# Kernel tuning notes

Measured on AMD Instinct MI355X. Metric: run time of the kernel, lower is better.

## Reference

```python
import jax, jax.numpy as jnp
import numpy as np

VOCAB = 32000
D = 256
B, S = 16, 128


def setup_inputs() -> dict:
    key = jax.random.key(0)
    ks = jax.random.split(key, 8)
    s = 1.0 / np.sqrt(D)
    return {
        "X": jax.random.randint(ks[0], (B, S), 0, VOCAB),
        "emb": jax.random.normal(ks[1], (VOCAB, D), dtype=jnp.float32),
        "Wl": jax.random.uniform(ks[2], (D, D), jnp.float32, -s, s),
        "bl": jax.random.uniform(ks[3], (D,), jnp.float32, -s, s),
        "Wr": jax.random.uniform(ks[4], (D, D), jnp.float32, -s, s),
        "br": jax.random.uniform(ks[5], (D,), jnp.float32, -s, s),
        "Wrel": jax.random.uniform(ks[6], (D, D), jnp.float32, -s, s),
        "brel": jax.random.uniform(ks[7], (D,), jnp.float32, -s, s),
    }


def reference(X, emb, Wl, bl, Wr, br, Wrel, brel):
    # X: [B,S] int -> embed [B,S,D]
    e = emb[X]
    L = jnp.einsum("bsd,de->bse", e, Wl.T) + bl  # left projection per token
    R = jnp.einsum("bsd,de->bse", e, Wr.T) + br  # right projection per token
    # all-pairs relu(L_i + R_j): [B,S,S,D]
    pair = jax.nn.relu(L[:, :, None, :] + R[:, None, :, :])
    # relation is affine, so mean over S^2 pairs commutes with it (same math,
    # one [B,D] GEMM instead of B*S^2 tiny ones)
    pooled = pair.mean(axis=(1, 2))  # [B,D]
    return pooled @ Wrel.T + brel
```

## Files before the change

kernel.cpp:

```cpp
#include <hip/hip_runtime.h>
#include <hip/hip_bf16.h>

#define DD 256
#define SS 128
#define BB 16

typedef __attribute__((ext_vector_type(8))) short bf16x8;
typedef __attribute__((ext_vector_type(4))) short bf16x4;
typedef __attribute__((ext_vector_type(4))) float f32x4;

static __device__ __forceinline__ short f2bf(float f) {
    __hip_bfloat16 h = __float2bfloat16(f);
    return *reinterpret_cast<short*>(&h);
}

static __device__ __forceinline__ int swz_off(int r, int kb) {
    return r * 512 + (kb ^ ((r & 7) << 4) ^ (((r >> 3) & 3) << 7));
}


__global__ __launch_bounds__(256) void k_proj(
    const int* __restrict__ X, const float* __restrict__ emb,
    const float* __restrict__ Wl, const float* __restrict__ bl,
    const float* __restrict__ Wr, const float* __restrict__ br,
    float* __restrict__ Lsd, float* __restrict__ Rsd,
    float* __restrict__ sumLp, float* __restrict__ sumRp)
{
    __shared__ __align__(16) short Ebf[64 * 256];
    __shared__ __align__(16) short Wbf[32 * 256];
    __shared__ float redw[4 * 16];
    __shared__ int toks[64];

    const int tid = threadIdx.x;
    const int bx  = blockIdx.x;
    const int tc  = bx >> 4;
    const int cc  = bx & 15;
    const int b   = tc >> 1;
    const int s0  = (tc & 1) * 64;
    const float* Wsrc = (cc < 8) ? Wl : Wr;
    const float* bsrc = (cc < 8) ? bl : br;
    const int dr0 = (cc & 7) * 32;

    if (tid < 64) toks[tid] = X[b * SS + s0 + tid];
    __syncthreads();

    char* Eb = (char*)Ebf;
    char* Wb = (char*)Wbf;

#pragma unroll
    for (int i = 0; i < 16; ++i) {
        int v = i * 256 + tid;
        int row = v >> 6, c4 = v & 63;
        float4 f = *(const float4*)&emb[(size_t)toks[row] * DD + c4 * 4];
        bf16x4 p; p[0] = f2bf(f.x); p[1] = f2bf(f.y); p[2] = f2bf(f.z); p[3] = f2bf(f.w);
        *(bf16x4*)(Eb + swz_off(row, c4 * 8)) = p;
    }
#pragma unroll
    for (int i = 0; i < 8; ++i) {
        int v = i * 256 + tid;
        int row = v >> 6, c4 = v & 63;
        float4 f = *(const float4*)&Wsrc[(size_t)(dr0 + row) * DD + c4 * 4];
        bf16x4 p; p[0] = f2bf(f.x); p[1] = f2bf(f.y); p[2] = f2bf(f.z); p[3] = f2bf(f.w);
        *(bf16x4*)(Wb + swz_off(row, c4 * 8)) = p;
    }
    __syncthreads();

    const int w    = tid >> 6;
    const int lane = tid & 63;
    const int wm = w >> 1, wn = w & 1;
    const int lr = lane & 15, lk = lane >> 4;

    f32x4 acc0 = {0.f, 0.f, 0.f, 0.f}, acc1 = acc0;
#pragma unroll
    for (int ks = 0; ks < 8; ++ks) {
        const int kb = ks * 64 + lk * 16;
        bf16x8 a0 = *(bf16x8*)(Eb + swz_off(wm * 32 + lr,      kb));
        bf16x8 a1 = *(bf16x8*)(Eb + swz_off(wm * 32 + 16 + lr, kb));
        bf16x8 b0 = *(bf16x8*)(Wb + swz_off(wn * 16 + lr,      kb));
        acc0 = __builtin_amdgcn_mfma_f32_16x16x32_bf16(a0, b0, acc0, 0, 0, 0);
        acc1 = __builtin_amdgcn_mfma_f32_16x16x32_bf16(a1, b0, acc1, 0, 0, 0);
    }

    const float bv = bsrc[dr0 + wn * 16 + lr];
    float* Tb = (cc < 8) ? Lsd : Rsd;
    const int dcol = dr0 + wn * 16 + lr;
#pragma unroll
    for (int reg = 0; reg < 4; ++reg) {
        int st = s0 + wm * 32 + lk * 4 + reg;
        Tb[((size_t)(b * SS) + st)      * DD + dcol] = acc0[reg] + bv;
        Tb[((size_t)(b * SS) + st + 16) * DD + dcol] = acc1[reg] + bv;
    }

    float t8 = (acc0[0] + acc0[1] + acc0[2] + acc0[3]) + bv * 8.0f
             + (acc1[0] + acc1[1] + acc1[2] + acc1[3]);
    t8 += __shfl_xor(t8, 16);
    t8 += __shfl_xor(t8, 32);
    if (lane < 16) redw[w * 16 + lr] = t8;
    __syncthreads();
    if (tid < 32) {
        int wn2 = tid >> 4, c = tid & 15;
        float s = redw[(0 * 2 + wn2) * 16 + c] + redw[(1 * 2 + wn2) * 16 + c];
        float* sp = (cc < 8) ? sumLp : sumRp;
        sp[(b * 2 + (tc & 1)) * DD + dr0 + wn2 * 16 + c] = s;
    }
}

__global__ __launch_bounds__(256) void k_pairs(
    const float* __restrict__ Lsd, const float* __restrict__ Rsd,
    float* __restrict__ absP)
{
    __shared__ float Ll[64 * 33];
    __shared__ float Rl[64 * 129];
    __shared__ float red[256];
    const int tid = threadIdx.x;
    const int bx  = blockIdx.x;
    const int b   = bx >> 4;
    const int dc  = (bx >> 2) & 3;
    const int is  = bx & 3;

#pragma unroll
    for (int it = 0; it < 2; ++it) {
        int v = it * 256 + tid;
        int srow = v >> 4, c4 = v & 15;
        float4 x = *(const float4*)&Lsd[((size_t)(b * SS) + is * 32 + srow) * DD + dc * 64 + c4 * 4];
        Ll[(c4 * 4 + 0) * 33 + srow] = x.x;
        Ll[(c4 * 4 + 1) * 33 + srow] = x.y;
        Ll[(c4 * 4 + 2) * 33 + srow] = x.z;
        Ll[(c4 * 4 + 3) * 33 + srow] = x.w;
    }
#pragma unroll
    for (int it = 0; it < 8; ++it) {
        int v = it * 256 + tid;
        int j = v >> 4, c4 = v & 15;
        float4 x = *(const float4*)&Rsd[((size_t)(b * SS) + j) * DD + dc * 64 + c4 * 4];
        Rl[(c4 * 4 + 0) * 129 + j] = x.x;
        Rl[(c4 * 4 + 1) * 129 + j] = x.y;
        Rl[(c4 * 4 + 2) * 129 + j] = x.z;
        Rl[(c4 * 4 + 3) * 129 + j] = x.w;
    }
    __syncthreads();

    const int dl = tid & 63;
    const int jg = tid >> 6;
    float rr[32];
#pragma unroll
    for (int j = 0; j < 32; ++j) rr[j] = Rl[dl * 129 + jg * 32 + j];

    float a0 = 0.f, a1 = 0.f, a2 = 0.f, a3 = 0.f;
#pragma unroll
    for (int i = 0; i < 32; ++i) {
        float l = Ll[dl * 33 + i];
#pragma unroll
        for (int j = 0; j < 32; j += 4) {
            a0 += fabsf(l + rr[j + 0]);
            a1 += fabsf(l + rr[j + 1]);
            a2 += fabsf(l + rr[j + 2]);
            a3 += fabsf(l + rr[j + 3]);
        }
    }
    red[tid] = (a0 + a1) + (a2 + a3);
    __syncthreads();
    if (tid < 64) {
        float s = red[tid] + red[tid + 64] + red[tid + 128] + red[tid + 192];
        absP[((b * 4 + dc) * 4 + is) * 64 + tid] = s;
    }
}

__global__ __launch_bounds__(256) void k_final(
    const float* __restrict__ sumLp, const float* __restrict__ sumRp,
    const float* __restrict__ absP,
    const float* __restrict__ Wrel, const float* __restrict__ brel,
    float* __restrict__ out)
{
    __shared__ float plds[DD];
    const int tid = threadIdx.x;
    const int b   = blockIdx.x;

    float sl = sumLp[(b * 2 + 0) * DD + tid] + sumLp[(b * 2 + 1) * DD + tid];
    float sr = sumRp[(b * 2 + 0) * DD + tid] + sumRp[(b * 2 + 1) * DD + tid];

    const int dc = tid >> 6, dl = tid & 63;
    float sa = 0.f;
#pragma unroll
    for (int is = 0; is < 4; ++is)
        sa += absP[((b * 4 + dc) * 4 + is) * 64 + dl];

    plds[tid] = (128.0f * (sl + sr) + sa) * (1.0f / 32768.0f);
    __syncthreads();

    float acc = brel[tid];
    const float4* w4 = (const float4*)(Wrel + (size_t)tid * DD);
#pragma unroll
    for (int k4 = 0; k4 < DD / 4; ++k4) {
        float4 p = *(float4*)&plds[k4 * 4];
        float4 w = w4[k4];
        acc = fmaf(p.x, w.x, acc);
        acc = fmaf(p.y, w.y, acc);
        acc = fmaf(p.z, w.z, acc);
        acc = fmaf(p.w, w.w, acc);
    }
    out[b * DD + tid] = acc;
}

extern "C" void kernel_launch(void* const* d_in, const int* in_sizes, int n_in,
                              void* d_out, int out_size, void* d_ws, size_t ws_size,
                              hipStream_t stream) {
    const int*   X    = (const int*)d_in[0];
    const float* emb  = (const float*)d_in[1];
    const float* Wl   = (const float*)d_in[2];
    const float* bl   = (const float*)d_in[3];
    const float* Wr   = (const float*)d_in[4];
    const float* br   = (const float*)d_in[5];
    const float* Wrel = (const float*)d_in[6];
    const float* brel = (const float*)d_in[7];
    float* out = (float*)d_out;

    float* ws = (float*)d_ws;
    float* Lsd   = ws;
    float* Rsd   = Lsd + (size_t)BB * SS * DD;
    float* sumLp = Rsd + (size_t)BB * SS * DD;
    float* sumRp = sumLp + BB * 2 * DD;
    float* absP  = sumRp + BB * 2 * DD;

    k_proj<<<512, 256, 0, stream>>>(X, emb, Wl, bl, Wr, br,
                                    Lsd, Rsd, sumLp, sumRp);
    k_pairs<<<256, 256, 0, stream>>>(Lsd, Rsd, absP);
    k_final<<<BB, 256, 0, stream>>>(sumLp, sumRp, absP, Wrel, brel, out);
}
```

Before: 29.63 us.

## Pre-convert embeddings and weights to bf16 once; store projections as bf16

Adds a conversion kernel that gathers the embedding rows and converts both projection weight matrices to bf16 in global memory once. k_proj then streams MFMA operands straight from global memory instead of having each of its 512 blocks re-convert fp32 data into swizzled LDS. The L/R projection outputs are stored as bf16, which halves the traffic into k_pairs. The cost is an extra kernel launch and lower precision in L/R for the abs-sum term.

```diff
diff --git a/kernel.cpp b/kernel.cpp
--- a/kernel.cpp
+++ b/kernel.cpp
@@ -6,89 +6,96 @@
 #define BB 16
 
 typedef __attribute__((ext_vector_type(8))) short bf16x8;
-typedef __attribute__((ext_vector_type(4))) short bf16x4;
 typedef __attribute__((ext_vector_type(4))) float f32x4;
 
 static __device__ __forceinline__ short f2bf(float f) {
     __hip_bfloat16 h = __float2bfloat16(f);
     return *reinterpret_cast<short*>(&h);
 }
-
-static __device__ __forceinline__ int swz_off(int r, int kb) {
-    return r * 512 + (kb ^ ((r & 7) << 4) ^ (((r >> 3) & 3) << 7));
-}
-
+static __device__ __forceinline__ float bf2f(short s) {
+    unsigned int u = ((unsigned int)(unsigned short)s) << 16;
+    return __uint_as_float(u);
+}
+
+
+__global__ __launch_bounds__(256) void k_conv(
+    const int* __restrict__ X, const float* __restrict__ emb,
+    const float* __restrict__ Wl, const float* __restrict__ Wr,
+    short* __restrict__ Ebfg, short* __restrict__ Wbfg)
+{
+    __shared__ int toksh[8];
+    const int tid = threadIdx.x;
+    const int bx  = blockIdx.x;
+    const int row = tid >> 5, g = tid & 31;
+
+    if (bx < 256) {
+        const int t0 = bx * 8;
+        if (tid < 8) toksh[tid] = X[t0 + tid];
+        __syncthreads();
+        const float* src = emb + (size_t)toksh[row] * DD + g * 8;
+        float4 f0 = *(const float4*)(src);
+        float4 f1 = *(const float4*)(src + 4);
+        bf16x8 p;
+        p[0]=f2bf(f0.x); p[1]=f2bf(f0.y); p[2]=f2bf(f0.z); p[3]=f2bf(f0.w);
+        p[4]=f2bf(f1.x); p[5]=f2bf(f1.y); p[6]=f2bf(f1.z); p[7]=f2bf(f1.w);
+        *(bf16x8*)(Ebfg + (size_t)(t0 + row) * DD + g * 8) = p;
+    } else {
+        const int w = (bx - 256) * 8 + row;
+        const float* src = ((w < 256) ? (Wl + (size_t)w * DD)
+                                      : (Wr + (size_t)(w - 256) * DD)) + g * 8;
+        float4 f0 = *(const float4*)(src);
+        float4 f1 = *(const float4*)(src + 4);
+        bf16x8 p;
+        p[0]=f2bf(f0.x); p[1]=f2bf(f0.y); p[2]=f2bf(f0.z); p[3]=f2bf(f0.w);
+        p[4]=f2bf(f1.x); p[5]=f2bf(f1.y); p[6]=f2bf(f1.z); p[7]=f2bf(f1.w);
+        *(bf16x8*)(Wbfg + (size_t)w * DD + g * 8) = p;
+    }
+}
 
 __global__ __launch_bounds__(256) void k_proj(
-    const int* __restrict__ X, const float* __restrict__ emb,
-    const float* __restrict__ Wl, const float* __restrict__ bl,
-    const float* __restrict__ Wr, const float* __restrict__ br,
-    float* __restrict__ Lsd, float* __restrict__ Rsd,
+    const short* __restrict__ Ebfg, const short* __restrict__ Wbfg,
+    const float* __restrict__ bl, const float* __restrict__ br,
+    short* __restrict__ Lsdh, short* __restrict__ Rsdh,
     float* __restrict__ sumLp, float* __restrict__ sumRp)
 {
-    __shared__ __align__(16) short Ebf[64 * 256];
-    __shared__ __align__(16) short Wbf[32 * 256];
     __shared__ float redw[4 * 16];
-    __shared__ int toks[64];
-
     const int tid = threadIdx.x;
     const int bx  = blockIdx.x;
     const int tc  = bx >> 4;
     const int cc  = bx & 15;
     const int b   = tc >> 1;
     const int s0  = (tc & 1) * 64;
-    const float* Wsrc = (cc < 8) ? Wl : Wr;
-    const float* bsrc = (cc < 8) ? bl : br;
+    const int t0  = tc * 64;
+    const int mat = cc >> 3;
     const int dr0 = (cc & 7) * 32;
-
-    if (tid < 64) toks[tid] = X[b * SS + s0 + tid];
-    __syncthreads();
-
-    char* Eb = (char*)Ebf;
-    char* Wb = (char*)Wbf;
-
-#pragma unroll
-    for (int i = 0; i < 16; ++i) {
-        int v = i * 256 + tid;
-        int row = v >> 6, c4 = v & 63;
-        float4 f = *(const float4*)&emb[(size_t)toks[row] * DD + c4 * 4];
-        bf16x4 p; p[0] = f2bf(f.x); p[1] = f2bf(f.y); p[2] = f2bf(f.z); p[3] = f2bf(f.w);
-        *(bf16x4*)(Eb + swz_off(row, c4 * 8)) = p;
-    }
-#pragma unroll
-    for (int i = 0; i < 8; ++i) {
-        int v = i * 256 + tid;
-        int row = v >> 6, c4 = v & 63;
-        float4 f = *(const float4*)&Wsrc[(size_t)(dr0 + row) * DD + c4 * 4];
-        bf16x4 p; p[0] = f2bf(f.x); p[1] = f2bf(f.y); p[2] = f2bf(f.z); p[3] = f2bf(f.w);
-        *(bf16x4*)(Wb + swz_off(row, c4 * 8)) = p;
-    }
-    __syncthreads();
 
     const int w    = tid >> 6;
     const int lane = tid & 63;
     const int wm = w >> 1, wn = w & 1;
     const int lr = lane & 15, lk = lane >> 4;
 
-    f32x4 acc0 = {0.f, 0.f, 0.f, 0.f}, acc1 = acc0;
+    const short* Arow0 = Ebfg + (size_t)(t0 + wm * 32 + lr) * DD + lk * 8;
+    const short* Arow1 = Arow0 + 16 * DD;
+    const short* Brow  = Wbfg + (size_t)(mat * 256 + dr0 + wn * 16 + lr) * DD + lk * 8;
+
+    f32x4 acc0 = {0.f,0.f,0.f,0.f}, acc1 = acc0;
 #pragma unroll
     for (int ks = 0; ks < 8; ++ks) {
-        const int kb = ks * 64 + lk * 16;
-        bf16x8 a0 = *(bf16x8*)(Eb + swz_off(wm * 32 + lr,      kb));
-        bf16x8 a1 = *(bf16x8*)(Eb + swz_off(wm * 32 + 16 + lr, kb));
-        bf16x8 b0 = *(bf16x8*)(Wb + swz_off(wn * 16 + lr,      kb));
+        bf16x8 a0 = *(const bf16x8*)(Arow0 + ks * 32);
+        bf16x8 a1 = *(const bf16x8*)(Arow1 + ks * 32);
+        bf16x8 b0 = *(const bf16x8*)(Brow  + ks * 32);
         acc0 = __builtin_amdgcn_mfma_f32_16x16x32_bf16(a0, b0, acc0, 0, 0, 0);
         acc1 = __builtin_amdgcn_mfma_f32_16x16x32_bf16(a1, b0, acc1, 0, 0, 0);
     }
 
-    const float bv = bsrc[dr0 + wn * 16 + lr];
-    float* Tb = (cc < 8) ? Lsd : Rsd;
+    const float bv = ((mat == 0) ? bl : br)[dr0 + wn * 16 + lr];
+    short* Tb = (mat == 0) ? Lsdh : Rsdh;
     const int dcol = dr0 + wn * 16 + lr;
 #pragma unroll
     for (int reg = 0; reg < 4; ++reg) {
         int st = s0 + wm * 32 + lk * 4 + reg;
-        Tb[((size_t)(b * SS) + st)      * DD + dcol] = acc0[reg] + bv;
-        Tb[((size_t)(b * SS) + st + 16) * DD + dcol] = acc1[reg] + bv;
+        Tb[((size_t)(b * SS) + st)      * DD + dcol] = f2bf(acc0[reg] + bv);
+        Tb[((size_t)(b * SS) + st + 16) * DD + dcol] = f2bf(acc1[reg] + bv);
     }
 
     float t8 = (acc0[0] + acc0[1] + acc0[2] + acc0[3]) + bv * 8.0f
@@ -100,13 +107,13 @@
     if (tid < 32) {
         int wn2 = tid >> 4, c = tid & 15;
         float s = redw[(0 * 2 + wn2) * 16 + c] + redw[(1 * 2 + wn2) * 16 + c];
-        float* sp = (cc < 8) ? sumLp : sumRp;
+        float* sp = (mat == 0) ? sumLp : sumRp;
         sp[(b * 2 + (tc & 1)) * DD + dr0 + wn2 * 16 + c] = s;
     }
 }
 
 __global__ __launch_bounds__(256) void k_pairs(
-    const float* __restrict__ Lsd, const float* __restrict__ Rsd,
+    const short* __restrict__ Lsdh, const short* __restrict__ Rsdh,
     float* __restrict__ absP)
 {
     __shared__ float Ll[64 * 33];
@@ -118,25 +125,19 @@
     const int dc  = (bx >> 2) & 3;
     const int is  = bx & 3;
 
-#pragma unroll
-    for (int it = 0; it < 2; ++it) {
+    {
+        int srow = tid >> 3, c8 = tid & 7;
+        bf16x8 x = *(const bf16x8*)&Lsdh[((size_t)(b * SS) + is * 32 + srow) * DD + dc * 64 + c8 * 8];
+#pragma unroll
+        for (int q = 0; q < 8; ++q) Ll[(c8 * 8 + q) * 33 + srow] = bf2f(x[q]);
+    }
+#pragma unroll
+    for (int it = 0; it < 4; ++it) {
         int v = it * 256 + tid;
-        int srow = v >> 4, c4 = v & 15;
-        float4 x = *(const float4*)&Lsd[((size_t)(b * SS) + is * 32 + srow) * DD + dc * 64 + c4 * 4];
-        Ll[(c4 * 4 + 0) * 33 + srow] = x.x;
-        Ll[(c4 * 4 + 1) * 33 + srow] = x.y;
-        Ll[(c4 * 4 + 2) * 33 + srow] = x.z;
-        Ll[(c4 * 4 + 3) * 33 + srow] = x.w;
-    }
-#pragma unroll
-    for (int it = 0; it < 8; ++it) {
-        int v = it * 256 + tid;
-        int j = v >> 4, c4 = v & 15;
-        float4 x = *(const float4*)&Rsd[((size_t)(b * SS) + j) * DD + dc * 64 + c4 * 4];
-        Rl[(c4 * 4 + 0) * 129 + j] = x.x;
-        Rl[(c4 * 4 + 1) * 129 + j] = x.y;
-        Rl[(c4 * 4 + 2) * 129 + j] = x.z;
-        Rl[(c4 * 4 + 3) * 129 + j] = x.w;
+        int j = v >> 3, c8 = v & 7;
+        bf16x8 x = *(const bf16x8*)&Rsdh[((size_t)(b * SS) + j) * DD + dc * 64 + c8 * 8];
+#pragma unroll
+        for (int q = 0; q < 8; ++q) Rl[(c8 * 8 + q) * 129 + j] = bf2f(x[q]);
     }
     __syncthreads();
 
@@ -215,15 +216,17 @@
     const float* brel = (const float*)d_in[7];
     float* out = (float*)d_out;
 
-    float* ws = (float*)d_ws;
-    float* Lsd   = ws;
-    float* Rsd   = Lsd + (size_t)BB * SS * DD;
-    float* sumLp = Rsd + (size_t)BB * SS * DD;
-    float* sumRp = sumLp + BB * 2 * DD;
-    float* absP  = sumRp + BB * 2 * DD;
-
-    k_proj<<<512, 256, 0, stream>>>(X, emb, Wl, bl, Wr, br,
-                                    Lsd, Rsd, sumLp, sumRp);
-    k_pairs<<<256, 256, 0, stream>>>(Lsd, Rsd, absP);
+    char* base = (char*)d_ws;
+    short* Ebfg  = (short*)(base);
+    short* Wbfg  = (short*)(base + (1u << 20));
+    short* Lsdh  = (short*)(base + 1310720);
+    short* Rsdh  = (short*)(base + 2359296);
+    float* sumLp = (float*)(base + 3407872);
+    float* sumRp = (float*)(base + 3440640);
+    float* absP  = (float*)(base + 3473408);
+
+    k_conv<<<320, 256, 0, stream>>>(X, emb, Wl, Wr, Ebfg, Wbfg);
+    k_proj<<<512, 256, 0, stream>>>(Ebfg, Wbfg, bl, br, Lsdh, Rsdh, sumLp, sumRp);
+    k_pairs<<<256, 256, 0, stream>>>(Lsdh, Rsdh, absP);
     k_final<<<BB, 256, 0, stream>>>(sumLp, sumRp, absP, Wrel, brel, out);
 }
```

Result: slower. 33.74 us (+13.9%).

## Fuse projection and pairwise abs-sum into one kernel, keep L/R in LDS

Applied to the files above, without the earlier changes.

Merges the projection kernel and the pairwise kernel into a single kernel. Each block takes one batch and a 16-column slice of D, computes both L and R for all 128 tokens with MFMA, and reduces the pairwise |L+R| sums directly from shared memory. The weight fragments are held in registers. This removes the global round trip for L/R and one kernel launch. In exchange, every block re-gathers and converts all 128 embedding rows, 16 times per batch, and the grid gets smaller at 256 blocks.

```diff
diff --git a/kernel.cpp b/kernel.cpp
--- a/kernel.cpp
+++ b/kernel.cpp
@@ -14,161 +14,129 @@
     return *reinterpret_cast<short*>(&h);
 }
 
-static __device__ __forceinline__ int swz_off(int r, int kb) {
-    return r * 512 + (kb ^ ((r & 7) << 4) ^ (((r >> 3) & 3) << 7));
+static __device__ __forceinline__ int swz(int r, int kb) {
+    return r * 512 + (kb ^ ((r & 7) << 4));
 }
 
 
-__global__ __launch_bounds__(256) void k_proj(
+__global__ __launch_bounds__(256) void k_fused(
     const int* __restrict__ X, const float* __restrict__ emb,
     const float* __restrict__ Wl, const float* __restrict__ bl,
     const float* __restrict__ Wr, const float* __restrict__ br,
-    float* __restrict__ Lsd, float* __restrict__ Rsd,
-    float* __restrict__ sumLp, float* __restrict__ sumRp)
+    float* __restrict__ sumLg, float* __restrict__ sumRg,
+    float* __restrict__ absS)
 {
     __shared__ __align__(16) short Ebf[64 * 256];
-    __shared__ __align__(16) short Wbf[32 * 256];
-    __shared__ float redw[4 * 16];
-    __shared__ int toks[64];
+    __shared__ __align__(16) float Lcol[16 * 132];
+    __shared__ __align__(16) float Rcol[16 * 132];
+    __shared__ float redA[256];
+    __shared__ float redR[256];
+    __shared__ float redL[16];
+    __shared__ int toksh[SS];
 
-    const int tid = threadIdx.x;
-    const int bx  = blockIdx.x;
-    const int tc  = bx >> 4;
-    const int cc  = bx & 15;
-    const int b   = tc >> 1;
-    const int s0  = (tc & 1) * 64;
-    const float* Wsrc = (cc < 8) ? Wl : Wr;
-    const float* bsrc = (cc < 8) ? bl : br;
-    const int dr0 = (cc & 7) * 32;
+    const int tid  = threadIdx.x;
+    const int b    = blockIdx.x >> 4;
+    const int dc   = blockIdx.x & 15;
+    const int dr0  = dc * 16;
+    const int w    = tid >> 6;
+    const int lane = tid & 63;
+    const int lr   = lane & 15, lk = lane >> 4;
 
-    if (tid < 64) toks[tid] = X[b * SS + s0 + tid];
+    bf16x8 wlf[8], wrf[8];
+    {
+        const float* plw = Wl + (size_t)(dr0 + lr) * DD + lk * 8;
+        const float* prw = Wr + (size_t)(dr0 + lr) * DD + lk * 8;
+#pragma unroll
+        for (int ks = 0; ks < 8; ++ks) {
+            float4 f0 = *(const float4*)(plw + ks * 32);
+            float4 f1 = *(const float4*)(plw + ks * 32 + 4);
+            bf16x8 p;
+            p[0]=f2bf(f0.x); p[1]=f2bf(f0.y); p[2]=f2bf(f0.z); p[3]=f2bf(f0.w);
+            p[4]=f2bf(f1.x); p[5]=f2bf(f1.y); p[6]=f2bf(f1.z); p[7]=f2bf(f1.w);
+            wlf[ks] = p;
+            f0 = *(const float4*)(prw + ks * 32);
+            f1 = *(const float4*)(prw + ks * 32 + 4);
+            p[0]=f2bf(f0.x); p[1]=f2bf(f0.y); p[2]=f2bf(f0.z); p[3]=f2bf(f0.w);
+            p[4]=f2bf(f1.x); p[5]=f2bf(f1.y); p[6]=f2bf(f1.z); p[7]=f2bf(f1.w);
+            wrf[ks] = p;
+        }
+    }
+
+    if (tid < SS) toksh[tid] = X[b * SS + tid];
+    const float blv = bl[dr0 + lr];
+    const float brv = br[dr0 + lr];
     __syncthreads();
 
     char* Eb = (char*)Ebf;
-    char* Wb = (char*)Wbf;
 
 #pragma unroll
-    for (int i = 0; i < 16; ++i) {
-        int v = i * 256 + tid;
-        int row = v >> 6, c4 = v & 63;
-        float4 f = *(const float4*)&emb[(size_t)toks[row] * DD + c4 * 4];
-        bf16x4 p; p[0] = f2bf(f.x); p[1] = f2bf(f.y); p[2] = f2bf(f.z); p[3] = f2bf(f.w);
-        *(bf16x4*)(Eb + swz_off(row, c4 * 8)) = p;
+    for (int h = 0; h < 2; ++h) {
+#pragma unroll
+        for (int i = 0; i < 16; ++i) {
+            int v = i * 256 + tid;
+            int row = v >> 6, c4 = v & 63;
+            float4 f = *(const float4*)&emb[(size_t)toksh[h * 64 + row] * DD + c4 * 4];
+            bf16x4 p; p[0]=f2bf(f.x); p[1]=f2bf(f.y); p[2]=f2bf(f.z); p[3]=f2bf(f.w);
+            *(bf16x4*)(Eb + swz(row, c4 * 8)) = p;
+        }
+        __syncthreads();
+
+        f32x4 accL = {0.f,0.f,0.f,0.f}, accR = accL;
+#pragma unroll
+        for (int ks = 0; ks < 8; ++ks) {
+            bf16x8 a = *(bf16x8*)(Eb + swz(w * 16 + lr, ks * 64 + lk * 16));
+            accL = __builtin_amdgcn_mfma_f32_16x16x32_bf16(a, wlf[ks], accL, 0, 0, 0);
+            accR = __builtin_amdgcn_mfma_f32_16x16x32_bf16(a, wrf[ks], accR, 0, 0, 0);
+        }
+#pragma unroll
+        for (int reg = 0; reg < 4; ++reg) {
+            int s = h * 64 + w * 16 + lk * 4 + reg;
+            Lcol[lr * 132 + s] = accL[reg] + blv;
+            Rcol[lr * 132 + s] = accR[reg] + brv;
+        }
+        __syncthreads();
     }
+
+    const int d = tid & 15, jg = tid >> 4;
+    float rr[8];
+    *(float4*)&rr[0] = *(float4*)&Rcol[d * 132 + jg * 8];
+    *(float4*)&rr[4] = *(float4*)&Rcol[d * 132 + jg * 8 + 4];
+    float srp = ((rr[0]+rr[1])+(rr[2]+rr[3])) + ((rr[4]+rr[5])+(rr[6]+rr[7]));
+
+    float sl = 0.f;
+    float a0 = 0.f, a1 = 0.f, a2 = 0.f, a3 = 0.f;
+    for (int i = 0; i < 128; i += 4) {
+        float4 l4 = *(float4*)&Lcol[d * 132 + i];
+        sl += (l4.x + l4.y) + (l4.z + l4.w);
 #pragma unroll
-    for (int i = 0; i < 8; ++i) {
-        int v = i * 256 + tid;
-        int row = v >> 6, c4 = v & 63;
-        float4 f = *(const float4*)&Wsrc[(size_t)(dr0 + row) * DD + c4 * 4];
-        bf16x4 p; p[0] = f2bf(f.x); p[1] = f2bf(f.y); p[2] = f2bf(f.z); p[3] = f2bf(f.w);
-        *(bf16x4*)(Wb + swz_off(row, c4 * 8)) = p;
+        for (int q = 0; q < 8; ++q) {
+            a0 += fabsf(l4.x + rr[q]);
+            a1 += fabsf(l4.y + rr[q]);
+            a2 += fabsf(l4.z + rr[q]);
+            a3 += fabsf(l4.w + rr[q]);
+        }
     }
+    redA[tid] = (a0 + a1) + (a2 + a3);
+    redR[tid] = srp;
+    if (jg == 0) redL[d] = sl;
     __syncthreads();
 
-    const int w    = tid >> 6;
-    const int lane = tid & 63;
-    const int wm = w >> 1, wn = w & 1;
-    const int lr = lane & 15, lk = lane >> 4;
-
-    f32x4 acc0 = {0.f, 0.f, 0.f, 0.f}, acc1 = acc0;
+    if (tid < 16) {
+        float sa = 0.f, sr = 0.f;
 #pragma unroll
-    for (int ks = 0; ks < 8; ++ks) {
-        const int kb = ks * 64 + lk * 16;
-        bf16x8 a0 = *(bf16x8*)(Eb + swz_off(wm * 32 + lr,      kb));
-        bf16x8 a1 = *(bf16x8*)(Eb + swz_off(wm * 32 + 16 + lr, kb));
-        bf16x8 b0 = *(bf16x8*)(Wb + swz_off(wn * 16 + lr,      kb));
-        acc0 = __builtin_amdgcn_mfma_f32_16x16x32_bf16(a0, b0, acc0, 0, 0, 0);
-        acc1 = __builtin_amdgcn_mfma_f32_16x16x32_bf16(a1, b0, acc1, 0, 0, 0);
-    }
-
-    const float bv = bsrc[dr0 + wn * 16 + lr];
-    float* Tb = (cc < 8) ? Lsd : Rsd;
-    const int dcol = dr0 + wn * 16 + lr;
-#pragma unroll
-    for (int reg = 0; reg < 4; ++reg) {
-        int st = s0 + wm * 32 + lk * 4 + reg;
-        Tb[((size_t)(b * SS) + st)      * DD + dcol] = acc0[reg] + bv;
-        Tb[((size_t)(b * SS) + st + 16) * DD + dcol] = acc1[reg] + bv;
-    }
-
-    float t8 = (acc0[0] + acc0[1] + acc0[2] + acc0[3]) + bv * 8.0f
-             + (acc1[0] + acc1[1] + acc1[2] + acc1[3]);
-    t8 += __shfl_xor(t8, 16);
-    t8 += __shfl_xor(t8, 32);
-    if (lane < 16) redw[w * 16 + lr] = t8;
-    __syncthreads();
-    if (tid < 32) {
-        int wn2 = tid >> 4, c = tid & 15;
-        float s = redw[(0 * 2 + wn2) * 16 + c] + redw[(1 * 2 + wn2) * 16 + c];
-        float* sp = (cc < 8) ? sumLp : sumRp;
-        sp[(b * 2 + (tc & 1)) * DD + dr0 + wn2 * 16 + c] = s;
-    }
-}
-
-__global__ __launch_bounds__(256) void k_pairs(
-    const float* __restrict__ Lsd, const float* __restrict__ Rsd,
-    float* __restrict__ absP)
-{
-    __shared__ float Ll[64 * 33];
-    __shared__ float Rl[64 * 129];
-    __shared__ float red[256];
-    const int tid = threadIdx.x;
-    const int bx  = blockIdx.x;
-    const int b   = bx >> 4;
-    const int dc  = (bx >> 2) & 3;
-    const int is  = bx & 3;
-
-#pragma unroll
-    for (int it = 0; it < 2; ++it) {
-        int v = it * 256 + tid;
-        int srow = v >> 4, c4 = v & 15;
-        float4 x = *(const float4*)&Lsd[((size_t)(b * SS) + is * 32 + srow) * DD + dc * 64 + c4 * 4];
-        Ll[(c4 * 4 + 0) * 33 + srow] = x.x;
-        Ll[(c4 * 4 + 1) * 33 + srow] = x.y;
-        Ll[(c4 * 4 + 2) * 33 + srow] = x.z;
-        Ll[(c4 * 4 + 3) * 33 + srow] = x.w;
-    }
-#pragma unroll
-    for (int it = 0; it < 8; ++it) {
-        int v = it * 256 + tid;
-        int j = v >> 4, c4 = v & 15;
-        float4 x = *(const float4*)&Rsd[((size_t)(b * SS) + j) * DD + dc * 64 + c4 * 4];
-        Rl[(c4 * 4 + 0) * 129 + j] = x.x;
-        Rl[(c4 * 4 + 1) * 129 + j] = x.y;
-        Rl[(c4 * 4 + 2) * 129 + j] = x.z;
-        Rl[(c4 * 4 + 3) * 129 + j] = x.w;
-    }
-    __syncthreads();
-
-    const int dl = tid & 63;
-    const int jg = tid >> 6;
-    float rr[32];
-#pragma unroll
-    for (int j = 0; j < 32; ++j) rr[j] = Rl[dl * 129 + jg * 32 + j];
-
-    float a0 = 0.f, a1 = 0.f, a2 = 0.f, a3 = 0.f;
-#pragma unroll
-    for (int i = 0; i < 32; ++i) {
-        float l = Ll[dl * 33 + i];
-#pragma unroll
-        for (int j = 0; j < 32; j += 4) {
-            a0 += fabsf(l + rr[j + 0]);
-            a1 += fabsf(l + rr[j + 1]);
-            a2 += fabsf(l + rr[j + 2]);
-            a3 += fabsf(l + rr[j + 3]);
+        for (int g = 0; g < 16; ++g) {
+            sa += redA[g * 16 + tid];
+            sr += redR[g * 16 + tid];
         }
-    }
-    red[tid] = (a0 + a1) + (a2 + a3);
-    __syncthreads();
-    if (tid < 64) {
-        float s = red[tid] + red[tid + 64] + red[tid + 128] + red[tid + 192];
-        absP[((b * 4 + dc) * 4 + is) * 64 + tid] = s;
+        absS [b * DD + dr0 + tid] = sa;
+        sumLg[b * DD + dr0 + tid] = redL[tid];
+        sumRg[b * DD + dr0 + tid] = sr;
     }
 }
 
 __global__ __launch_bounds__(256) void k_final(
-    const float* __restrict__ sumLp, const float* __restrict__ sumRp,
-    const float* __restrict__ absP,
+    const float* __restrict__ sumLg, const float* __restrict__ sumRg,
+    const float* __restrict__ absS,
     const float* __restrict__ Wrel, const float* __restrict__ brel,
     float* __restrict__ out)
 {
@@ -176,14 +144,9 @@
     const int tid = threadIdx.x;
     const int b   = blockIdx.x;
 
-    float sl = sumLp[(b * 2 + 0) * DD + tid] + sumLp[(b * 2 + 1) * DD + tid];
-    float sr = sumRp[(b * 2 + 0) * DD + tid] + sumRp[(b * 2 + 1) * DD + tid];
-
-    const int dc = tid >> 6, dl = tid & 63;
-    float sa = 0.f;
-#pragma unroll
-    for (int is = 0; is < 4; ++is)
-        sa += absP[((b * 4 + dc) * 4 + is) * 64 + dl];
+    float sl = sumLg[b * DD + tid];
+    float sr = sumRg[b * DD + tid];
+    float sa = absS [b * DD + tid];
 
     plds[tid] = (128.0f * (sl + sr) + sa) * (1.0f / 32768.0f);
     __syncthreads();
@@ -215,15 +178,12 @@
     const float* brel = (const float*)d_in[7];
     float* out = (float*)d_out;
 
-    float* ws = (float*)d_ws;
-    float* Lsd   = ws;
-    float* Rsd   = Lsd + (size_t)BB * SS * DD;
-    float* sumLp = Rsd + (size_t)BB * SS * DD;
-    float* sumRp = sumLp + BB * 2 * DD;
-    float* absP  = sumRp + BB * 2 * DD;
+    float* ws    = (float*)d_ws;
+    float* sumLg = ws;
+    float* sumRg = sumLg + BB * DD;
+    float* absS  = sumRg + BB * DD;
 
-    k_proj<<<512, 256, 0, stream>>>(X, emb, Wl, bl, Wr, br,
-                                    Lsd, Rsd, sumLp, sumRp);
-    k_pairs<<<256, 256, 0, stream>>>(Lsd, Rsd, absP);
-    k_final<<<BB, 256, 0, stream>>>(sumLp, sumRp, absP, Wrel, brel, out);
+    k_fused<<<BB * 16, 256, 0, stream>>>(X, emb, Wl, bl, Wr, br,
+                                         sumLg, sumRg, absS);
+    k_final<<<BB, 256, 0, stream>>>(sumLg, sumRg, absS, Wrel, brel, out);
 }
```

Measured after the change: 31.79 us. 7.3% more time.
